# Optimization experiments

Hardware: AMD Instinct MI355X
Metric: run time of the kernel (lower is better)

Reference implementation:

```python
import jax, jax.numpy as jnp
import numpy as np

N, E, DIN, H, H1, H2, B, DEC = 20000, 320000, 128, 4, 64, 32, 4096, 512


def _seg_softmax(e, seg, n):
    # numerically stable softmax over edges grouped by destination node
    m = jax.ops.segment_max(e, seg, num_segments=n)
    p = jnp.exp(e - m[seg])
    s = jax.ops.segment_sum(p, seg, num_segments=n)
    return p / (s[seg] + 1e-16)


def _prelu(x, a):
    return jnp.where(x >= 0, x, a * x)


def _gat(x, src, dst, n, w, a_src, a_dst, b, concat):
    # PyG GATConv: shared linear, additive attention, leaky_relu(0.2), softmax per dst
    h_, c = a_src.shape
    h = (x @ w).reshape(-1, h_, c)                      # [n, H, C]
    al = jnp.einsum('nhc,hc->nh', h, a_src)[src] + jnp.einsum('nhc,hc->nh', h, a_dst)[dst]
    alpha = _seg_softmax(jax.nn.leaky_relu(al, 0.2), dst, n)  # [e, H]
    out = jax.ops.segment_sum(alpha[..., None] * h[src], dst, num_segments=n)
    out = out.reshape(n, h_ * c) if concat else out.mean(1)
    return out + b


def _gt(x, src, dst, n, wq, bq, wk, bk, wv, bv, ws, bs, heads, concat):
    # PyG TransformerConv: scaled dot-product attention over edges + root skip
    c = wq.shape[1] // heads
    q = (x @ wq + bq).reshape(-1, heads, c)
    k = (x @ wk + bk).reshape(-1, heads, c)
    v = (x @ wv + bv).reshape(-1, heads, c)
    e = (q[dst] * k[src]).sum(-1) / jnp.sqrt(jnp.float32(c))  # [e, heads]
    alpha = _seg_softmax(e, dst, n)
    agg = jax.ops.segment_sum(alpha[..., None] * v[src], dst, num_segments=n)
    agg = agg.reshape(n, heads * c) if concat else agg.mean(1)
    return agg + x @ ws + bs


def _forward(fl, edge_index, idx):
    (x_o, x_a, gat1_w, gat1_asrc, gat1_adst, gat1_b, gat2_w, gat2_asrc, gat2_adst, gat2_b,
     pg1, pg2, gt1_wq, gt1_bq, gt1_wk, gt1_bk, gt1_wv, gt1_bv, gt1_ws, gt1_bs,
     gt2_wq, gt2_bq, gt2_wk, gt2_bk, gt2_wv, gt2_bv, gt2_ws, gt2_bs, pt1, pt2,
     fuse_w, fuse_b, mlp1_w, mlp1_b, disc_w, disc_b,
     fus_w1, fus_b1, fus_w2, fus_b2, fus_w3, fus_b3, adv_w, adv_b) = fl
    n = x_o.shape[0]
    src, dst = edge_index[0], edge_index[1]
    # GATConv adds self loops by default; TransformerConv does not
    loop = jnp.arange(n, dtype=src.dtype)
    src_g = jnp.concatenate([src, loop])
    dst_g = jnp.concatenate([dst, loop])

    def branch_gat(x):
        x1 = _prelu(_gat(x, src_g, dst_g, n, gat1_w, gat1_asrc, gat1_adst, gat1_b, True), pg1)
        return _prelu(_gat(x1, src_g, dst_g, n, gat2_w, gat2_asrc, gat2_adst, gat2_b, False), pg2)

    def branch_gt(x):
        x1 = _prelu(_gt(x, src, dst, n, gt1_wq, gt1_bq, gt1_wk, gt1_bk, gt1_wv, gt1_bv, gt1_ws, gt1_bs, H, True), pt1)
        return _prelu(_gt(x1, src, dst, n, gt2_wq, gt2_bq, gt2_wk, gt2_bk, gt2_wv, gt2_bv, gt2_ws, gt2_bs, 1, False), pt2)

    x2_o = jnp.concatenate([branch_gat(x_o), branch_gt(x_o)], 1) @ fuse_w + fuse_b
    x2_a = jnp.concatenate([branch_gat(x_a), branch_gt(x_a)], 1) @ fuse_w + fuse_b

    def summary(z):
        return jax.nn.sigmoid(z.mean(0)) @ mlp1_w + mlp1_b   # [H2]

    h_os, h_os_a = summary(x2_o), summary(x2_a)

    def disc(cvec, hp, hm):
        # Bilinear(n_h, n_h, 1): sc = h W c^T + b
        s1 = (hp @ disc_w) @ cvec + disc_b[0]
        s2 = (hm @ disc_w) @ cvec + disc_b[0]
        return jnp.stack([s1, s2], 1)                       # [N, 2]

    ret_os = disc(h_os, x2_o, x2_a)
    ret_os_a = disc(h_os_a, x2_a, x2_o)

    # default task_type: direct indexing of node embeddings
    hcat = jnp.concatenate([x2_o[idx[0]], x2_o[idx[1]]], 1)  # [B, 2*H2]
    hh = jax.nn.relu(hcat @ fus_w1 + fus_b1)
    log = hh @ fus_w2 + fus_b2
    log1 = hh @ fus_w3 + fus_b3

    sc1 = (x2_o @ adv_w + adv_b).sum(1)[None, :]
    sc2 = (x2_a @ adv_w + adv_b).sum(1)[None, :]
    logits = jnp.concatenate([sc1, sc2], 1)                  # [1, 2N]
    return (log, ret_os, ret_os_a, x2_o, logits, log1)


_SHAPES = {
    'x_o': (N, DIN), 'x_a': (N, DIN),
    'gat1_w': (DIN, H * H1), 'gat1_asrc': (H, H1), 'gat1_adst': (H, H1), 'gat1_b': (H * H1,),
    'gat2_w': (H * H1, H2), 'gat2_asrc': (1, H2), 'gat2_adst': (1, H2), 'gat2_b': (H2,),
    'pg1': (H * H1,), 'pg2': (H2,),
    'gt1_wq': (DIN, H * H1), 'gt1_bq': (H * H1,), 'gt1_wk': (DIN, H * H1), 'gt1_bk': (H * H1,),
    'gt1_wv': (DIN, H * H1), 'gt1_bv': (H * H1,), 'gt1_ws': (DIN, H * H1), 'gt1_bs': (H * H1,),
    'gt2_wq': (H * H1, H2), 'gt2_bq': (H2,), 'gt2_wk': (H * H1, H2), 'gt2_bk': (H2,),
    'gt2_wv': (H * H1, H2), 'gt2_bv': (H2,), 'gt2_ws': (H * H1, H2), 'gt2_bs': (H2,),
    'pt1': (H * H1,), 'pt2': (H2,),
    'fuse_w': (2 * H2, H2), 'fuse_b': (H2,),
    'mlp1_w': (H2, H2), 'mlp1_b': (H2,),
    'disc_w': (H2, H2), 'disc_b': (1,),
    'fus_w1': (2 * H2, DEC), 'fus_b1': (DEC,), 'fus_w2': (DEC, 2), 'fus_b2': (2,),
    'fus_w3': (DEC, 2), 'fus_b3': (2,),
    'adv_w': (H2, H2), 'adv_b': (H2,),
}


def setup_inputs() -> dict:
    key = jax.random.key(0)
    inp = {}
    for i, (name, shp) in enumerate(_SHAPES.items()):
        inp[name] = jax.random.normal(jax.random.fold_in(key, i), shp, jnp.float32) * 0.05
    inp['edge_index'] = jax.random.randint(jax.random.fold_in(key, 100), (2, E), 0, N, dtype=jnp.int32)
    inp['idx'] = jax.random.randint(jax.random.fold_in(key, 101), (2, B), 0, N, dtype=jnp.int32)
    return inp


def reference(x_o, x_a, gat1_w, gat1_asrc, gat1_adst, gat1_b, gat2_w, gat2_asrc, gat2_adst, gat2_b,
              pg1, pg2, gt1_wq, gt1_bq, gt1_wk, gt1_bk, gt1_wv, gt1_bv, gt1_ws, gt1_bs,
              gt2_wq, gt2_bq, gt2_wk, gt2_bk, gt2_wv, gt2_bv, gt2_ws, gt2_bs, pt1, pt2,
              fuse_w, fuse_b, mlp1_w, mlp1_b, disc_w, disc_b,
              fus_w1, fus_b1, fus_w2, fus_b2, fus_w3, fus_b3, adv_w, adv_b,
              edge_index, idx):
    fl = (x_o, x_a, gat1_w, gat1_asrc, gat1_adst, gat1_b, gat2_w, gat2_asrc, gat2_adst, gat2_b,
          pg1, pg2, gt1_wq, gt1_bq, gt1_wk, gt1_bk, gt1_wv, gt1_bv, gt1_ws, gt1_bs,
          gt2_wq, gt2_bq, gt2_wk, gt2_bk, gt2_wv, gt2_bv, gt2_ws, gt2_bs, pt1, pt2,
          fuse_w, fuse_b, mlp1_w, mlp1_b, disc_w, disc_b,
          fus_w1, fus_b1, fus_w2, fus_b2, fus_w3, fus_b3, adv_w, adv_b)
    return _forward(fl, edge_index, idx)
```

## Files before the change

kernel.cpp:

```cpp
#include <hip/hip_runtime.h>
#include <math.h>

#define NN 20000
#define NE 320000
#define NB 4096

typedef unsigned short u16;
typedef unsigned char u8;
typedef __attribute__((ext_vector_type(8))) short short8;
typedef __attribute__((ext_vector_type(4))) float f32x4;
typedef __attribute__((ext_vector_type(2))) float f32x2;

#define FP8_SCALE 16.0f
#define FP8_INV 0.0625f
#define LOG2E 1.44269504088896341f

__device__ __forceinline__ float b2f(u16 u) {
  unsigned int x = ((unsigned int)u) << 16;
  return __uint_as_float(x);
}
__device__ __forceinline__ u16 f2b(float f) {
  unsigned int x = __float_as_uint(f);
  return (u16)((x + 0x7fffu + ((x >> 16) & 1u)) >> 16);
}
__device__ __forceinline__ float q2f(u8 b) {
  f32x2 v = __builtin_amdgcn_cvt_pk_f32_fp8((int)b, false);
  return v[0];
}
__device__ __forceinline__ void q4(unsigned int u, float* f) {
  f32x2 lo = __builtin_amdgcn_cvt_pk_f32_fp8((int)u, false);
  f32x2 hi = __builtin_amdgcn_cvt_pk_f32_fp8((int)u, true);
  f[0] = lo[0]; f[1] = lo[1]; f[2] = hi[0]; f[3] = hi[1];
}
template <int CTRL>
__device__ __forceinline__ float dppadd(float x) {
  int y = __builtin_amdgcn_update_dpp(0, __float_as_int(x), CTRL, 0xf, 0xf, true);
  return x + __int_as_float(y);
}
__device__ __forceinline__ float red16(float x) {
  x = dppadd<0xB1>(x);
  x = dppadd<0x4E>(x);
  x = dppadd<0x124>(x);
  x = dppadd<0x128>(x);
  return x;
}


__global__ void k_pack1(const float* __restrict__ w0, const float* __restrict__ w1,
                        const float* __restrict__ w2, const float* __restrict__ w3,
                        const float* __restrict__ w4, const float* __restrict__ b1,
                        const float* __restrict__ b2, const float* __restrict__ b3,
                        const float* __restrict__ b4, u16* __restrict__ Wt,
                        float* __restrict__ bp) {
  int t = blockIdx.x * blockDim.x + threadIdx.x;
  if (t < 1280 * 128) {
    int j = t >> 7, k = t & 127;
    int seg = j >> 8, jj = j & 255;
    const float* s = (seg == 0) ? w0 : (seg == 1) ? w1 : (seg == 2) ? w2 : (seg == 3) ? w3 : w4;
    Wt[t] = f2b(s[k * 256 + jj]);
  }
  if (t < 1280) {
    int seg = t >> 8, jj = t & 255;
    bp[t] = (seg == 0) ? 0.0f : (seg == 1) ? b1[jj] : (seg == 2) ? b2[jj] : (seg == 3) ? b3[jj] : b4[jj];
  }
}

__global__ void k_pack2(const float* __restrict__ wq, const float* __restrict__ wk,
                        const float* __restrict__ wv, const float* __restrict__ ws,
                        const float* __restrict__ wg, const float* __restrict__ bq,
                        const float* __restrict__ bk, const float* __restrict__ bv,
                        const float* __restrict__ bs, u16* __restrict__ Wt,
                        float* __restrict__ bp) {
  int t = blockIdx.x * blockDim.x + threadIdx.x;
  if (t < 160 * 256) {
    int j = t >> 8, k = t & 255;
    int seg = j >> 5, jj = j & 31;
    const float* s = (seg == 0) ? wq : (seg == 1) ? wk : (seg == 2) ? wv : (seg == 3) ? ws : wg;
    Wt[t] = f2b(s[k * 32 + jj]);
  }
  if (t < 160) {
    int seg = t >> 5, jj = t & 31;
    bp[t] = (seg == 0) ? bq[jj] : (seg == 1) ? bk[jj] : (seg == 2) ? bv[jj] : (seg == 3) ? bs[jj] : 0.0f;
  }
}

__global__ void k_tobf16x2(const float* __restrict__ xo, const float* __restrict__ xa,
                           u16* __restrict__ bo, u16* __restrict__ ba) {
  int t = blockIdx.x * blockDim.x + threadIdx.x;
  if (t >= 2 * NN * 128) return;
  if (t < NN * 128) bo[t] = f2b(xo[t]);
  else ba[t - NN * 128] = f2b(xa[t - NN * 128]);
}


__global__ void k_hist(const int* __restrict__ dst, int* __restrict__ deg) {
  int t = blockIdx.x * blockDim.x + threadIdx.x;
  if (t < NE) atomicAdd(&deg[dst[t]], 1);
}

__global__ void k_scan20000(const int* __restrict__ deg, int* __restrict__ offs,
                            int* __restrict__ cur) {
  __shared__ int part[1024];
  int t = threadIdx.x;
  int loc[20];
  int s = 0;
#pragma unroll
  for (int i = 0; i < 20; ++i) {
    int idx = t * 20 + i;
    int v = (idx < NN) ? deg[idx] : 0;
    loc[i] = s;
    s += v;
  }
  part[t] = s;
  __syncthreads();
  for (int off = 1; off < 1024; off <<= 1) {
    int v = (t >= off) ? part[t - off] : 0;
    __syncthreads();
    part[t] += v;
    __syncthreads();
  }
  int base = (t > 0) ? part[t - 1] : 0;
#pragma unroll
  for (int i = 0; i < 20; ++i) {
    int idx = t * 20 + i;
    if (idx < NN) {
      offs[idx] = base + loc[i];
      cur[idx] = base + loc[i];
    }
  }
  if (t == 1023) offs[NN] = part[1023];
}

__global__ void k_scatter(const int* __restrict__ src, const int* __restrict__ dst,
                          int* __restrict__ cur, int* __restrict__ esrcs) {
  int t = blockIdx.x * blockDim.x + threadIdx.x;
  if (t >= NE) return;
  int d = dst[t];
  int pos = atomicAdd(&cur[d], 1);
  esrcs[pos] = src[t];
}


template <int LAYER>
__global__ void k_mfma_gemm_s(const u16* __restrict__ A0, const u16* __restrict__ A1,
                              int asel, const u16* __restrict__ Bt,
                              const float* __restrict__ bias, int M, int K, int Nc,
                              u8* __restrict__ G, u16* __restrict__ Cb) {
  const u16* A = (blockIdx.x >= (unsigned)asel) ? A1 : A0;
  int m0 = blockIdx.y * 128, n0 = blockIdx.x * 128;
  int wid = threadIdx.x >> 6, lane = threadIdx.x & 63;
  int mw = m0 + (wid & 1) * 64, nw = n0 + (wid >> 1) * 64;
  int arow = mw + (lane & 15);
  int bcol = nw + (lane & 15);
  int kblk = (lane >> 4) * 8;
  f32x4 acc[4][4] = {};
  const short8 zero8 = {0, 0, 0, 0, 0, 0, 0, 0};
  for (int k0 = 0; k0 < K; k0 += 32) {
    short8 af[4], bf[4];
#pragma unroll
    for (int mf = 0; mf < 4; ++mf) {
      int r = arow + mf * 16;
      if (r > M - 1) r = M - 1;
      af[mf] = *reinterpret_cast<const short8*>(&A[(size_t)r * K + k0 + kblk]);
    }
#pragma unroll
    for (int nf = 0; nf < 4; ++nf) {
      int c = bcol + nf * 16;
      bf[nf] = (c < Nc) ? *reinterpret_cast<const short8*>(&Bt[(size_t)c * K + k0 + kblk])
                        : zero8;
    }
#pragma unroll
    for (int mf = 0; mf < 4; ++mf)
#pragma unroll
      for (int nf = 0; nf < 4; ++nf)
        acc[mf][nf] = __builtin_amdgcn_mfma_f32_16x16x32_bf16(bf[nf], af[mf],
                                                              acc[mf][nf], 0, 0, 0);
  }
  const int CSTR = (LAYER == 1) ? 512 : 64;
  const int GSTR = (LAYER == 1) ? 768 : 96;
#pragma unroll
  for (int mf = 0; mf < 4; ++mf) {
    int row = mw + mf * 16 + (lane & 15);
    if (row >= M) continue;
#pragma unroll
    for (int nf = 0; nf < 4; ++nf) {
      int col0 = nw + nf * 16 + ((lane >> 4) << 2);
      if (col0 >= Nc) continue;
      float4 bs4 = *reinterpret_cast<const float4*>(&bias[col0]);
      float v0 = acc[mf][nf][0] + bs4.x;
      float v1 = acc[mf][nf][1] + bs4.y;
      float v2 = acc[mf][nf][2] + bs4.z;
      float v3 = acc[mf][nf][3] + bs4.w;
      int seg = (LAYER == 1) ? (col0 >> 8) : (col0 >> 5);
      bool tobf = (LAYER == 1) ? (seg == 1 || seg == 4) : (seg == 0 || seg == 3);
      if (tobf) {
        int ccol = (LAYER == 1) ? ((seg == 1) ? col0 - 256 : col0 - 768)
                                : ((seg == 0) ? col0 : col0 - 64);
        ushort4 w4;
        w4.x = f2b(v0); w4.y = f2b(v1); w4.z = f2b(v2); w4.w = f2b(v3);
        *reinterpret_cast<ushort4*>(&Cb[(size_t)row * CSTR + ccol]) = w4;
      } else {
        int gcol = (LAYER == 1) ? ((seg == 0) ? col0 : col0 - 256)
                                : ((seg == 4) ? col0 - 64 : col0 - 32);
        unsigned int p = (unsigned int)__builtin_amdgcn_cvt_pk_fp8_f32(
            v0 * FP8_SCALE, v1 * FP8_SCALE, 0, false);
        p = (unsigned int)__builtin_amdgcn_cvt_pk_fp8_f32(
            v2 * FP8_SCALE, v3 * FP8_SCALE, (int)p, true);
        *reinterpret_cast<unsigned int*>(&G[(size_t)row * GSTR + gcol]) = p;
      }
    }
  }
}


__global__ void k_gat_al8(const u8* __restrict__ h, int stride, int coff,
                          const float* __restrict__ asrc, const float* __restrict__ adst,
                          float* __restrict__ als, float* __restrict__ ald, int total,
                          int heads, int c) {
  int i = blockIdx.x * blockDim.x + threadIdx.x;
  if (i >= total) return;
  int node = i / heads, hd = i - node * heads;
  const u8* hp = h + (size_t)node * stride + coff + hd * c;
  const float* as = asrc + hd * c;
  const float* ad = adst + hd * c;
  float s1 = 0.0f, s2 = 0.0f;
  for (int k = 0; k < c; k += 4) {
    float f[4];
    q4(*reinterpret_cast<const unsigned int*>(&hp[k]), f);
#pragma unroll
    for (int j = 0; j < 4; ++j) {
      s1 = fmaf(f[j], as[k + j], s1);
      s2 = fmaf(f[j], ad[k + j], s2);
    }
  }
  als[i] = s1 * (FP8_INV * LOG2E);
  ald[i] = s2 * (FP8_INV * LOG2E);
}

__global__ void k_agg256_fused(const int* __restrict__ offs, const int* __restrict__ esrcs,
                               const float* __restrict__ als, const float* __restrict__ ald,
                               const u8* __restrict__ G8, const u16* __restrict__ C1b,
                               const float* __restrict__ gbias,
                               const float* __restrict__ pg, const float* __restrict__ pt,
                               u16* __restrict__ outG, u16* __restrict__ outT) {
  int d = blockIdx.x * 4 + (threadIdx.x >> 6);
  if (d >= NN) return;
  int lane = threadIdx.x & 63;
  int head = lane >> 4, c4 = lane << 2;
  ushort4 q4v = *reinterpret_cast<const ushort4*>(&C1b[(size_t)d * 512 + c4]);
  float q0 = b2f(q4v.x), q1 = b2f(q4v.y), q2 = b2f(q4v.z), q3 = b2f(q4v.w);
  float aldd = ald[d * 4 + head];
  float ga0 = 0, ga1 = 0, ga2 = 0, ga3 = 0, gden = 0.0f;
  float ta0 = 0, ta1 = 0, ta2 = 0, ta3 = 0, tden = 1e-16f;
  int b0 = offs[d], b1 = offs[d + 1];
  const float GTC = 0.125f * FP8_INV * LOG2E;
  unsigned int f0 = 0, k0 = 0, v0 = 0, f1 = 0, k1 = 0, v1 = 0;
  float al0 = 0.0f, al1 = 0.0f;
  if (b0 < b1) {
    int s = esrcs[b0];
    const u8* row = &G8[(size_t)s * 768];
    f0 = *reinterpret_cast<const unsigned int*>(&row[c4]);
    k0 = *reinterpret_cast<const unsigned int*>(&row[256 + c4]);
    v0 = *reinterpret_cast<const unsigned int*>(&row[512 + c4]);
    al0 = als[s * 4 + head];
  }
  if (b0 + 1 < b1) {
    int s = esrcs[b0 + 1];
    const u8* row = &G8[(size_t)s * 768];
    f1 = *reinterpret_cast<const unsigned int*>(&row[c4]);
    k1 = *reinterpret_cast<const unsigned int*>(&row[256 + c4]);
    v1 = *reinterpret_cast<const unsigned int*>(&row[512 + c4]);
    al1 = als[s * 4 + head];
  }
  for (int i = b0; i < b1; ++i) {
    unsigned int f2_ = 0, k2_ = 0, v2_ = 0;
    float al2_ = 0.0f;
    if (i + 2 < b1) {
      int s = esrcs[i + 2];
      const u8* row = &G8[(size_t)s * 768];
      f2_ = *reinterpret_cast<const unsigned int*>(&row[c4]);
      k2_ = *reinterpret_cast<const unsigned int*>(&row[256 + c4]);
      v2_ = *reinterpret_cast<const unsigned int*>(&row[512 + c4]);
      al2_ = als[s * 4 + head];
    }
    float kf[4];
    q4(k0, kf);
    float pp = q0 * kf[0];
    pp = fmaf(q1, kf[1], pp);
    pp = fmaf(q2, kf[2], pp);
    pp = fmaf(q3, kf[3], pp);
    pp = red16(pp);
    float pet = exp2f(pp * GTC);
    float v = al0 + aldd;
    float peg = exp2f(v >= 0.0f ? v : 0.2f * v);
    float ff[4], vf[4];
    q4(f0, ff);
    q4(v0, vf);
    ga0 = fmaf(peg, ff[0], ga0);
    ga1 = fmaf(peg, ff[1], ga1);
    ga2 = fmaf(peg, ff[2], ga2);
    ga3 = fmaf(peg, ff[3], ga3);
    gden += peg;
    ta0 = fmaf(pet, vf[0], ta0);
    ta1 = fmaf(pet, vf[1], ta1);
    ta2 = fmaf(pet, vf[2], ta2);
    ta3 = fmaf(pet, vf[3], ta3);
    tden += pet;
    f0 = f1; k0 = k1; v0 = v1; al0 = al1;
    f1 = f2_; k1 = k2_; v1 = v2_; al1 = al2_;
  }
  {
    float v = als[d * 4 + head] + aldd;
    float pe = exp2f(v >= 0.0f ? v : 0.2f * v);
    float ff[4];
    q4(*reinterpret_cast<const unsigned int*>(&G8[(size_t)d * 768 + c4]), ff);
    ga0 = fmaf(pe, ff[0], ga0);
    ga1 = fmaf(pe, ff[1], ga1);
    ga2 = fmaf(pe, ff[2], ga2);
    ga3 = fmaf(pe, ff[3], ga3);
    gden += pe;
  }
  float ig = FP8_INV / gden, it = FP8_INV / tden;
  float o0 = ga0 * ig + gbias[c4 + 0];
  float o1 = ga1 * ig + gbias[c4 + 1];
  float o2 = ga2 * ig + gbias[c4 + 2];
  float o3 = ga3 * ig + gbias[c4 + 3];
  o0 = o0 >= 0.0f ? o0 : pg[c4 + 0] * o0;
  o1 = o1 >= 0.0f ? o1 : pg[c4 + 1] * o1;
  o2 = o2 >= 0.0f ? o2 : pg[c4 + 2] * o2;
  o3 = o3 >= 0.0f ? o3 : pg[c4 + 3] * o3;
  ushort4 wg4;
  wg4.x = f2b(o0); wg4.y = f2b(o1); wg4.z = f2b(o2); wg4.w = f2b(o3);
  *reinterpret_cast<ushort4*>(&outG[(size_t)d * 256 + c4]) = wg4;
  ushort4 sk = *reinterpret_cast<const ushort4*>(&C1b[(size_t)d * 512 + 256 + c4]);
  float u0 = ta0 * it + b2f(sk.x);
  float u1 = ta1 * it + b2f(sk.y);
  float u2 = ta2 * it + b2f(sk.z);
  float u3 = ta3 * it + b2f(sk.w);
  u0 = u0 >= 0.0f ? u0 : pt[c4 + 0] * u0;
  u1 = u1 >= 0.0f ? u1 : pt[c4 + 1] * u1;
  u2 = u2 >= 0.0f ? u2 : pt[c4 + 2] * u2;
  u3 = u3 >= 0.0f ? u3 : pt[c4 + 3] * u3;
  ushort4 wt4;
  wt4.x = f2b(u0); wt4.y = f2b(u1); wt4.z = f2b(u2); wt4.w = f2b(u3);
  *reinterpret_cast<ushort4*>(&outT[(size_t)d * 256 + c4]) = wt4;
}

__global__ void k_agg32_fuse(const int* __restrict__ offs, const int* __restrict__ esrcs,
                             const float* __restrict__ als, const float* __restrict__ ald,
                             const u8* __restrict__ G28, const u16* __restrict__ C2b,
                             const float* __restrict__ gbias,
                             const float* __restrict__ pg, const float* __restrict__ pt,
                             const float* __restrict__ fw, const float* __restrict__ fb,
                             float* __restrict__ x2out, float* __restrict__ colsum) {
  __shared__ float xgv[8][32], xtv[8][32];
  int g = threadIdx.x >> 5, l = threadIdx.x & 31;
  int d = blockIdx.x * 8 + g;
  float qv = b2f(C2b[(size_t)d * 64 + l]);
  float aldd = ald[d];
  float ga = 0.0f, gden = 0.0f;
  float ta = 0.0f, tden = 1e-16f;
  int b0 = offs[d], b1 = offs[d + 1];
  const float GTC2 = 0.17677669529663687f * FP8_INV * LOG2E;
  u8 kc = 0, vc = 0, hc = 0;
  float alc = 0;
  if (b0 < b1) {
    int sc = esrcs[b0];
    const u8* row = &G28[(size_t)sc * 96];
    kc = row[l]; vc = row[32 + l]; hc = row[64 + l];
    alc = als[sc];
  }
  for (int i = b0; i < b1; ++i) {
    u8 kn = kc, vn = vc, hn = hc;
    float aln = alc;
    if (i + 1 < b1) {
      int sn = esrcs[i + 1];
      const u8* row = &G28[(size_t)sn * 96];
      kn = row[l]; vn = row[32 + l]; hn = row[64 + l];
      aln = als[sn];
    }
    float pp = qv * q2f(kc);
    pp = red16(pp);
    pp += __shfl_xor(pp, 16, 32);
    float pet = exp2f(pp * GTC2);
    float v = alc + aldd;
    float peg = exp2f(v >= 0.0f ? v : 0.2f * v);
    ga = fmaf(peg, q2f(hc), ga);
    gden += peg;
    ta = fmaf(pet, q2f(vc), ta);
    tden += pet;
    kc = kn; vc = vn; hc = hn; alc = aln;
  }
  {
    float v = als[d] + aldd;
    float pe = exp2f(v >= 0.0f ? v : 0.2f * v);
    ga = fmaf(pe, q2f(G28[(size_t)d * 96 + 64 + l]), ga);
    gden += pe;
  }
  float og = ga * FP8_INV / gden + gbias[l];
  og = og >= 0.0f ? og : pg[l] * og;
  float ot = ta * FP8_INV / tden + b2f(C2b[(size_t)d * 64 + 32 + l]);
  ot = ot >= 0.0f ? ot : pt[l] * ot;
  xgv[g][l] = og;
  xtv[g][l] = ot;
  __syncthreads();
  float acc = fb[l];
#pragma unroll
  for (int i = 0; i < 32; ++i) {
    acc = fmaf(xgv[g][i], fw[i * 32 + l], acc);
    acc = fmaf(xtv[g][i], fw[(32 + i) * 32 + l], acc);
  }
  x2out[(size_t)d * 32 + l] = acc;
  __syncthreads();
  xgv[g][l] = acc;
  __syncthreads();
  if (g == 0) {
    float s = acc;
#pragma unroll
    for (int i = 1; i < 8; ++i) s += xgv[i][l];
    atomicAdd(&colsum[(blockIdx.x & 7) * 32 + l], s);
  }
}


__global__ void k_disc_all(const float* __restrict__ x2o, const float* __restrict__ x2a_,
                           const float* __restrict__ cso, const float* __restrict__ csa,
                           const float* __restrict__ mlp_w, const float* __restrict__ mlp_b,
                           const float* __restrict__ disc_w, const float* __restrict__ db,
                           float* __restrict__ ret_os, float* __restrict__ ret_os_a) {
  __shared__ float sgv[64], h1s[32], h2s[32], m1[32], m2[32];
  int t = threadIdx.x;
  if (t < 64) {
    int j = t & 31;
    const float* cs = (t < 32) ? cso : csa;
    float m = 0.0f;
#pragma unroll
    for (int i = 0; i < 8; ++i) m += cs[i * 32 + j];
    sgv[t] = 1.0f / (1.0f + expf(-m / (float)NN));
  }
  __syncthreads();
  if (t < 64) {
    int j = t & 31;
    const float* sg = (t < 32) ? sgv : sgv + 32;
    float acc = mlp_b[j];
#pragma unroll
    for (int i = 0; i < 32; ++i) acc = fmaf(sg[i], mlp_w[i * 32 + j], acc);
    (t < 32 ? h1s : h2s)[j] = acc;
  }
  __syncthreads();
  if (t < 64) {
    int k = t & 31;
    const float* hv = (t < 32) ? h1s : h2s;
    float acc = 0.0f;
#pragma unroll
    for (int i = 0; i < 32; ++i) acc = fmaf(disc_w[k * 32 + i], hv[i], acc);
    (t < 32 ? m1 : m2)[k] = acc;
  }
  __syncthreads();
  int n = blockIdx.x * blockDim.x + t;
  if (n >= NN) return;
  const float* a = x2o + (size_t)n * 32;
  const float* b = x2a_ + (size_t)n * 32;
  float s_oo = 0, s_ao = 0, s_aa = 0, s_oa = 0;
#pragma unroll
  for (int i = 0; i < 32; ++i) {
    float v1 = m1[i], v2 = m2[i];
    s_oo = fmaf(a[i], v1, s_oo);
    s_ao = fmaf(b[i], v1, s_ao);
    s_aa = fmaf(b[i], v2, s_aa);
    s_oa = fmaf(a[i], v2, s_oa);
  }
  float bb = db[0];
  ret_os[n * 2 + 0] = s_oo + bb;
  ret_os[n * 2 + 1] = s_ao + bb;
  ret_os_a[n * 2 + 0] = s_aa + bb;
  ret_os_a[n * 2 + 1] = s_oa + bb;
}

__global__ void k_dec1(const float* __restrict__ x2o, const int* __restrict__ idx0,
                       const int* __restrict__ idx1, const float* __restrict__ w,
                       const float* __restrict__ b1, float* __restrict__ hh) {
  int t = blockIdx.x * blockDim.x + threadIdx.x;
  if (t >= NB * 512) return;
  int bb = t >> 9, n = t & 511;
  const float* r0 = x2o + (size_t)idx0[bb] * 32;
  const float* r1 = x2o + (size_t)idx1[bb] * 32;
  float acc = b1[n];
#pragma unroll
  for (int i = 0; i < 32; ++i) acc = fmaf(r0[i], w[i * 512 + n], acc);
#pragma unroll
  for (int i = 0; i < 32; ++i) acc = fmaf(r1[i], w[(32 + i) * 512 + n], acc);
  hh[t] = fmaxf(acc, 0.0f);
}

__global__ void k_dec2w(const float* __restrict__ hh, const float* __restrict__ w2,
                        const float* __restrict__ b2, const float* __restrict__ w3,
                        const float* __restrict__ b3, float* __restrict__ logo,
                        float* __restrict__ log1) {
  int wv = (blockIdx.x * blockDim.x + threadIdx.x) >> 6;
  int lane = threadIdx.x & 63;
  if (wv >= NB * 4) return;
  int bb = wv >> 2, j = wv & 3;
  const float* h = hh + (size_t)bb * 512;
  const float* ws = (j < 2) ? w2 : w3;
  int jj = j & 1;
  float acc = 0.0f;
#pragma unroll
  for (int k = 0; k < 8; ++k) acc = fmaf(h[lane + k * 64], ws[(lane + k * 64) * 2 + jj], acc);
  acc += __shfl_xor(acc, 32);
  acc += __shfl_xor(acc, 16);
  acc += __shfl_xor(acc, 8);
  acc += __shfl_xor(acc, 4);
  acc += __shfl_xor(acc, 2);
  acc += __shfl_xor(acc, 1);
  if (lane == 0) {
    float b = (j < 2) ? b2[jj] : b3[jj];
    ((j < 2) ? logo : log1)[bb * 2 + jj] = acc + b;
  }
}

__global__ void k_adv(const float* __restrict__ x2o, const float* __restrict__ x2a,
                      const float* __restrict__ aw, const float* __restrict__ ab,
                      float* __restrict__ logits) {
  __shared__ float sadv[33];
  int t = threadIdx.x;
  if (t < 32) {
    float s = 0.0f;
#pragma unroll
    for (int j = 0; j < 32; ++j) s += aw[t * 32 + j];
    sadv[t] = s;
  } else if (t == 32) {
    float s = 0.0f;
#pragma unroll
    for (int j = 0; j < 32; ++j) s += ab[j];
    sadv[32] = s;
  }
  __syncthreads();
  int n = blockIdx.x * blockDim.x + t;
  if (n >= 2 * NN) return;
  const float* row = (n < NN) ? (x2o + (size_t)n * 32) : (x2a + (size_t)(n - NN) * 32);
  float acc = sadv[32];
#pragma unroll
  for (int i = 0; i < 32; ++i) acc = fmaf(row[i], sadv[i], acc);
  logits[n] = acc;
}


extern "C" void kernel_launch(void* const* d_in, const int* in_sizes, int n_in,
                              void* d_out, int out_size, void* d_ws, size_t ws_size,
                              hipStream_t stream) {
  const float* x_o = (const float*)d_in[0];
  const float* x_a = (const float*)d_in[1];
  const float* gat1_w = (const float*)d_in[2];
  const float* gat1_asrc = (const float*)d_in[3];
  const float* gat1_adst = (const float*)d_in[4];
  const float* gat1_b = (const float*)d_in[5];
  const float* gat2_w = (const float*)d_in[6];
  const float* gat2_asrc = (const float*)d_in[7];
  const float* gat2_adst = (const float*)d_in[8];
  const float* gat2_b = (const float*)d_in[9];
  const float* pg1 = (const float*)d_in[10];
  const float* pg2 = (const float*)d_in[11];
  const float* gt1_wq = (const float*)d_in[12];
  const float* gt1_bq = (const float*)d_in[13];
  const float* gt1_wk = (const float*)d_in[14];
  const float* gt1_bk = (const float*)d_in[15];
  const float* gt1_wv = (const float*)d_in[16];
  const float* gt1_bv = (const float*)d_in[17];
  const float* gt1_ws = (const float*)d_in[18];
  const float* gt1_bs = (const float*)d_in[19];
  const float* gt2_wq = (const float*)d_in[20];
  const float* gt2_bq = (const float*)d_in[21];
  const float* gt2_wk = (const float*)d_in[22];
  const float* gt2_bk = (const float*)d_in[23];
  const float* gt2_wv = (const float*)d_in[24];
  const float* gt2_bv = (const float*)d_in[25];
  const float* gt2_ws = (const float*)d_in[26];
  const float* gt2_bs = (const float*)d_in[27];
  const float* pt1 = (const float*)d_in[28];
  const float* pt2 = (const float*)d_in[29];
  const float* fuse_w = (const float*)d_in[30];
  const float* fuse_b = (const float*)d_in[31];
  const float* mlp1_w = (const float*)d_in[32];
  const float* mlp1_b = (const float*)d_in[33];
  const float* disc_w = (const float*)d_in[34];
  const float* disc_b = (const float*)d_in[35];
  const float* fus_w1 = (const float*)d_in[36];
  const float* fus_b1 = (const float*)d_in[37];
  const float* fus_w2 = (const float*)d_in[38];
  const float* fus_b2 = (const float*)d_in[39];
  const float* fus_w3 = (const float*)d_in[40];
  const float* fus_b3 = (const float*)d_in[41];
  const float* adv_w = (const float*)d_in[42];
  const float* adv_b = (const float*)d_in[43];
  const int* ei = (const int*)d_in[44];
  const int* idxp = (const int*)d_in[45];
  const int* esrc = ei;
  const int* edst = ei + NE;
  const int* idx0 = idxp;
  const int* idx1 = idxp + NB;

  float* w = (float*)d_ws;
  size_t o = 0;
  u8* G8 = (u8*)(w + o); o += 3840000;
  u16* C1b = (u16*)(w + o); o += 5120000;
  u8* G28 = (u8*)(w + o); o += 480000;
  u16* C2b = (u16*)(w + o); o += 640000;
  u16* bufB = (u16*)(w + o); o += 2560000;
  u16* bufE = (u16*)(w + o); o += 2560000;
  u16* xb_o = (u16*)(w + o); o += 1280000;
  u16* xb_a = (u16*)(w + o); o += 1280000;
  u16* Wt1 = (u16*)(w + o); o += 81920;
  u16* Wt2 = (u16*)(w + o); o += 20480;
  float* bp1 = w + o; o += 1280;
  float* bp2 = w + o; o += 160;
  float* als = w + o; o += NN * 4;
  float* ald = w + o; o += NN * 4;
  float* x2a = w + o; o += NN * 32;
  float* hh = w + o; o += NB * 512;
  int* deg = (int*)(w + o); o += NN;
  int* offs = (int*)(w + o); o += NN + 8;
  int* cur = (int*)(w + o); o += NN;
  int* esrcs = (int*)(w + o); o += NE;
  float* colsum_o = w + o; o += 256;
  float* colsum_a = w + o; o += 256;

  float* out = (float*)d_out;
  float* out_log = out;
  float* out_ret = out + 8192;
  float* out_reta = out + 48192;
  float* out_x2o = out + 88192;
  float* out_logit = out + 728192;
  float* out_log1 = out + 768192;

  k_pack1<<<(1280 * 128 + 255) / 256, 256, 0, stream>>>(gat1_w, gt1_wq, gt1_wk, gt1_wv,
                                                        gt1_ws, gt1_bq, gt1_bk, gt1_bv,
                                                        gt1_bs, Wt1, bp1);
  k_pack2<<<(160 * 256 + 255) / 256, 256, 0, stream>>>(gt2_wq, gt2_wk, gt2_wv, gt2_ws,
                                                       gat2_w, gt2_bq, gt2_bk, gt2_bv,
                                                       gt2_bs, Wt2, bp2);
  k_tobf16x2<<<(2 * NN * 128 + 255) / 256, 256, 0, stream>>>(x_o, x_a, xb_o, xb_a);
  hipMemsetAsync(deg, 0, NN * sizeof(int), stream);
  hipMemsetAsync(colsum_o, 0, 512 * sizeof(float), stream);
  k_hist<<<(NE + 255) / 256, 256, 0, stream>>>(edst, deg);
  k_scan20000<<<1, 1024, 0, stream>>>(deg, offs, cur);
  k_scatter<<<(NE + 255) / 256, 256, 0, stream>>>(esrc, edst, cur, esrcs);

  auto branch = [&](const u16* xb, float* x2out, float* colsum) {
    {
      dim3 g(10, (NN + 127) / 128);
      k_mfma_gemm_s<1><<<g, 256, 0, stream>>>(xb, xb, 999, Wt1, bp1, NN, 128, 1280,
                                              G8, C1b);
    }
    k_gat_al8<<<(NN * 4 + 255) / 256, 256, 0, stream>>>(G8, 768, 0, gat1_asrc, gat1_adst,
                                                        als, ald, NN * 4, 4, 64);
    k_agg256_fused<<<NN / 4, 256, 0, stream>>>(offs, esrcs, als, ald, G8, C1b,
                                               gat1_b, pg1, pt1, bufB, bufE);
    {
      dim3 g(2, (NN + 127) / 128);
      k_mfma_gemm_s<2><<<g, 256, 0, stream>>>(bufE, bufB, 1, Wt2, bp2, NN, 256, 160,
                                              G28, C2b);
    }
    k_gat_al8<<<(NN + 255) / 256, 256, 0, stream>>>(G28, 96, 64, gat2_asrc, gat2_adst,
                                                    als, ald, NN, 1, 32);
    k_agg32_fuse<<<NN / 8, 256, 0, stream>>>(offs, esrcs, als, ald, G28, C2b,
                                             gat2_b, pg2, pt2, fuse_w, fuse_b,
                                             x2out, colsum);
  };

  branch(xb_o, out_x2o, colsum_o);
  branch(xb_a, x2a, colsum_a);

  k_disc_all<<<(NN + 255) / 256, 256, 0, stream>>>(out_x2o, x2a, colsum_o, colsum_a,
                                                   mlp1_w, mlp1_b, disc_w, disc_b,
                                                   out_ret, out_reta);
  k_dec1<<<(NB * 512 + 255) / 256, 256, 0, stream>>>(out_x2o, idx0, idx1, fus_w1,
                                                     fus_b1, hh);
  k_dec2w<<<(NB * 4 * 64 + 255) / 256, 256, 0, stream>>>(hh, fus_w2, fus_b2, fus_w3,
                                                         fus_b3, out_log, out_log1);
  k_adv<<<(2 * NN + 255) / 256, 256, 0, stream>>>(out_x2o, x2a, adv_w, adv_b, out_logit);
}
```

Baseline: 464.4 us.

## Split edge aggregation across two waves per node and fuse tail kernels

The 256-wide aggregation kernel now assigns two wavefronts to each destination node. Each wave processes alternate edges, and the partial sums are combined through shared memory. This doubles the parallelism and memory-level concurrency on the gather-bound edge loop, at the cost of a block barrier and some LDS traffic. Separately, the adversarial logits are folded into the discriminator kernel, and the two decoder kernels are merged into one per-batch-row kernel that keeps the hidden layer in shared memory, removing two launches and the global hh buffer.

```diff
diff --git a/kernel.cpp b/kernel.cpp
--- a/kernel.cpp
+++ b/kernel.cpp
@@ -243,40 +243,43 @@
                                const float* __restrict__ gbias,
                                const float* __restrict__ pg, const float* __restrict__ pt,
                                u16* __restrict__ outG, u16* __restrict__ outT) {
-  int d = blockIdx.x * 4 + (threadIdx.x >> 6);
-  if (d >= NN) return;
+  __shared__ float part[2][64][10];
+  int g = threadIdx.x >> 6;
+  int dl = g >> 1, half = g & 1;
+  int d = blockIdx.x * 2 + dl;
   int lane = threadIdx.x & 63;
   int head = lane >> 4, c4 = lane << 2;
   ushort4 q4v = *reinterpret_cast<const ushort4*>(&C1b[(size_t)d * 512 + c4]);
   float q0 = b2f(q4v.x), q1 = b2f(q4v.y), q2 = b2f(q4v.z), q3 = b2f(q4v.w);
   float aldd = ald[d * 4 + head];
   float ga0 = 0, ga1 = 0, ga2 = 0, ga3 = 0, gden = 0.0f;
-  float ta0 = 0, ta1 = 0, ta2 = 0, ta3 = 0, tden = 1e-16f;
-  int b0 = offs[d], b1 = offs[d + 1];
+  float ta0 = 0, ta1 = 0, ta2 = 0, ta3 = 0;
+  float tden = half ? 0.0f : 1e-16f;
+  int bs = offs[d] + half, be = offs[d + 1];
   const float GTC = 0.125f * FP8_INV * LOG2E;
   unsigned int f0 = 0, k0 = 0, v0 = 0, f1 = 0, k1 = 0, v1 = 0;
   float al0 = 0.0f, al1 = 0.0f;
-  if (b0 < b1) {
-    int s = esrcs[b0];
+  if (bs < be) {
+    int s = esrcs[bs];
     const u8* row = &G8[(size_t)s * 768];
     f0 = *reinterpret_cast<const unsigned int*>(&row[c4]);
     k0 = *reinterpret_cast<const unsigned int*>(&row[256 + c4]);
     v0 = *reinterpret_cast<const unsigned int*>(&row[512 + c4]);
     al0 = als[s * 4 + head];
   }
-  if (b0 + 1 < b1) {
-    int s = esrcs[b0 + 1];
+  if (bs + 2 < be) {
+    int s = esrcs[bs + 2];
     const u8* row = &G8[(size_t)s * 768];
     f1 = *reinterpret_cast<const unsigned int*>(&row[c4]);
     k1 = *reinterpret_cast<const unsigned int*>(&row[256 + c4]);
     v1 = *reinterpret_cast<const unsigned int*>(&row[512 + c4]);
     al1 = als[s * 4 + head];
   }
-  for (int i = b0; i < b1; ++i) {
+  for (int i = bs; i < be; i += 2) {
     unsigned int f2_ = 0, k2_ = 0, v2_ = 0;
     float al2_ = 0.0f;
-    if (i + 2 < b1) {
-      int s = esrcs[i + 2];
+    if (i + 4 < be) {
+      int s = esrcs[i + 4];
       const u8* row = &G8[(size_t)s * 768];
       f2_ = *reinterpret_cast<const unsigned int*>(&row[c4]);
       k2_ = *reinterpret_cast<const unsigned int*>(&row[256 + c4]);
@@ -309,7 +312,7 @@
     f0 = f1; k0 = k1; v0 = v1; al0 = al1;
     f1 = f2_; k1 = k2_; v1 = v2_; al1 = al2_;
   }
-  {
+  if (half == 0) {
     float v = als[d * 4 + head] + aldd;
     float pe = exp2f(v >= 0.0f ? v : 0.2f * v);
     float ff[4];
@@ -320,6 +323,16 @@
     ga3 = fmaf(pe, ff[3], ga3);
     gden += pe;
   }
+  if (half == 1) {
+    float* p = part[dl][lane];
+    p[0] = ga0; p[1] = ga1; p[2] = ga2; p[3] = ga3; p[4] = gden;
+    p[5] = ta0; p[6] = ta1; p[7] = ta2; p[8] = ta3; p[9] = tden;
+  }
+  __syncthreads();
+  if (half == 1) return;
+  const float* p = part[dl][lane];
+  ga0 += p[0]; ga1 += p[1]; ga2 += p[2]; ga3 += p[3]; gden += p[4];
+  ta0 += p[5]; ta1 += p[6]; ta2 += p[7]; ta3 += p[8]; tden += p[9];
   float ig = FP8_INV / gden, it = FP8_INV / tden;
   float o0 = ga0 * ig + gbias[c4 + 0];
   float o1 = ga1 * ig + gbias[c4 + 1];
@@ -427,8 +440,10 @@
                            const float* __restrict__ cso, const float* __restrict__ csa,
                            const float* __restrict__ mlp_w, const float* __restrict__ mlp_b,
                            const float* __restrict__ disc_w, const float* __restrict__ db,
-                           float* __restrict__ ret_os, float* __restrict__ ret_os_a) {
-  __shared__ float sgv[64], h1s[32], h2s[32], m1[32], m2[32];
+                           const float* __restrict__ aw, const float* __restrict__ ab,
+                           float* __restrict__ ret_os, float* __restrict__ ret_os_a,
+                           float* __restrict__ logits) {
+  __shared__ float sgv[64], h1s[32], h2s[32], m1[32], m2[32], sadv[33];
   int t = threadIdx.x;
   if (t < 64) {
     int j = t & 31;
@@ -438,6 +453,18 @@
     for (int i = 0; i < 8; ++i) m += cs[i * 32 + j];
     sgv[t] = 1.0f / (1.0f + expf(-m / (float)NN));
   }
+  if (t >= 64 && t < 96) {
+    int j = t & 31;
+    float s = 0.0f;
+#pragma unroll
+    for (int i = 0; i < 32; ++i) s += aw[j * 32 + i];
+    sadv[j] = s;
+  } else if (t == 96) {
+    float s = 0.0f;
+#pragma unroll
+    for (int i = 0; i < 32; ++i) s += ab[i];
+    sadv[32] = s;
+  }
   __syncthreads();
   if (t < 64) {
     int j = t & 31;
@@ -462,51 +489,54 @@
   const float* a = x2o + (size_t)n * 32;
   const float* b = x2a_ + (size_t)n * 32;
   float s_oo = 0, s_ao = 0, s_aa = 0, s_oa = 0;
+  float lo = sadv[32], la = sadv[32];
 #pragma unroll
   for (int i = 0; i < 32; ++i) {
-    float v1 = m1[i], v2 = m2[i];
-    s_oo = fmaf(a[i], v1, s_oo);
-    s_ao = fmaf(b[i], v1, s_ao);
-    s_aa = fmaf(b[i], v2, s_aa);
-    s_oa = fmaf(a[i], v2, s_oa);
+    float v1 = m1[i], v2 = m2[i], av = sadv[i];
+    float ai = a[i], bi = b[i];
+    s_oo = fmaf(ai, v1, s_oo);
+    s_ao = fmaf(bi, v1, s_ao);
+    s_aa = fmaf(bi, v2, s_aa);
+    s_oa = fmaf(ai, v2, s_oa);
+    lo = fmaf(ai, av, lo);
+    la = fmaf(bi, av, la);
   }
   float bb = db[0];
   ret_os[n * 2 + 0] = s_oo + bb;
   ret_os[n * 2 + 1] = s_ao + bb;
   ret_os_a[n * 2 + 0] = s_aa + bb;
   ret_os_a[n * 2 + 1] = s_oa + bb;
-}
-
-__global__ void k_dec1(const float* __restrict__ x2o, const int* __restrict__ idx0,
-                       const int* __restrict__ idx1, const float* __restrict__ w,
-                       const float* __restrict__ b1, float* __restrict__ hh) {
-  int t = blockIdx.x * blockDim.x + threadIdx.x;
-  if (t >= NB * 512) return;
-  int bb = t >> 9, n = t & 511;
+  logits[n] = lo;
+  logits[NN + n] = la;
+}
+
+__global__ void k_dec(const float* __restrict__ x2o, const int* __restrict__ idx0,
+                      const int* __restrict__ idx1, const float* __restrict__ w1,
+                      const float* __restrict__ b1, const float* __restrict__ w2,
+                      const float* __restrict__ b2, const float* __restrict__ w3,
+                      const float* __restrict__ b3, float* __restrict__ logo,
+                      float* __restrict__ log1) {
+  __shared__ float hhs[512];
+  int bb = blockIdx.x;
   const float* r0 = x2o + (size_t)idx0[bb] * 32;
   const float* r1 = x2o + (size_t)idx1[bb] * 32;
-  float acc = b1[n];
-#pragma unroll
-  for (int i = 0; i < 32; ++i) acc = fmaf(r0[i], w[i * 512 + n], acc);
-#pragma unroll
-  for (int i = 0; i < 32; ++i) acc = fmaf(r1[i], w[(32 + i) * 512 + n], acc);
-  hh[t] = fmaxf(acc, 0.0f);
-}
-
-__global__ void k_dec2w(const float* __restrict__ hh, const float* __restrict__ w2,
-                        const float* __restrict__ b2, const float* __restrict__ w3,
-                        const float* __restrict__ b3, float* __restrict__ logo,
-                        float* __restrict__ log1) {
-  int wv = (blockIdx.x * blockDim.x + threadIdx.x) >> 6;
-  int lane = threadIdx.x & 63;
-  if (wv >= NB * 4) return;
-  int bb = wv >> 2, j = wv & 3;
-  const float* h = hh + (size_t)bb * 512;
-  const float* ws = (j < 2) ? w2 : w3;
-  int jj = j & 1;
+  int t = threadIdx.x;
+  for (int n = t; n < 512; n += 256) {
+    float acc = b1[n];
+#pragma unroll
+    for (int i = 0; i < 32; ++i) {
+      acc = fmaf(r0[i], w1[i * 512 + n], acc);
+      acc = fmaf(r1[i], w1[(32 + i) * 512 + n], acc);
+    }
+    hhs[n] = fmaxf(acc, 0.0f);
+  }
+  __syncthreads();
+  int g = t >> 6, lane = t & 63;
+  const float* ws = (g < 2) ? w2 : w3;
+  int jj = g & 1;
   float acc = 0.0f;
 #pragma unroll
-  for (int k = 0; k < 8; ++k) acc = fmaf(h[lane + k * 64], ws[(lane + k * 64) * 2 + jj], acc);
+  for (int k = 0; k < 8; ++k) acc = fmaf(hhs[lane + k * 64], ws[(lane + k * 64) * 2 + jj], acc);
   acc += __shfl_xor(acc, 32);
   acc += __shfl_xor(acc, 16);
   acc += __shfl_xor(acc, 8);
@@ -514,35 +544,9 @@
   acc += __shfl_xor(acc, 2);
   acc += __shfl_xor(acc, 1);
   if (lane == 0) {
-    float b = (j < 2) ? b2[jj] : b3[jj];
-    ((j < 2) ? logo : log1)[bb * 2 + jj] = acc + b;
-  }
-}
-
-__global__ void k_adv(const float* __restrict__ x2o, const float* __restrict__ x2a,
-                      const float* __restrict__ aw, const float* __restrict__ ab,
-                      float* __restrict__ logits) {
-  __shared__ float sadv[33];
-  int t = threadIdx.x;
-  if (t < 32) {
-    float s = 0.0f;
-#pragma unroll
-    for (int j = 0; j < 32; ++j) s += aw[t * 32 + j];
-    sadv[t] = s;
-  } else if (t == 32) {
-    float s = 0.0f;
-#pragma unroll
-    for (int j = 0; j < 32; ++j) s += ab[j];
-    sadv[32] = s;
-  }
-  __syncthreads();
-  int n = blockIdx.x * blockDim.x + t;
-  if (n >= 2 * NN) return;
-  const float* row = (n < NN) ? (x2o + (size_t)n * 32) : (x2a + (size_t)(n - NN) * 32);
-  float acc = sadv[32];
-#pragma unroll
-  for (int i = 0; i < 32; ++i) acc = fmaf(row[i], sadv[i], acc);
-  logits[n] = acc;
+    float b = (g < 2) ? b2[jj] : b3[jj];
+    ((g < 2) ? logo : log1)[bb * 2 + jj] = acc + b;
+  }
 }
 
 
@@ -617,7 +621,6 @@
   float* als = w + o; o += NN * 4;
   float* ald = w + o; o += NN * 4;
   float* x2a = w + o; o += NN * 32;
-  float* hh = w + o; o += NB * 512;
   int* deg = (int*)(w + o); o += NN;
   int* offs = (int*)(w + o); o += NN + 8;
   int* cur = (int*)(w + o); o += NN;
@@ -654,7 +657,7 @@
     }
     k_gat_al8<<<(NN * 4 + 255) / 256, 256, 0, stream>>>(G8, 768, 0, gat1_asrc, gat1_adst,
                                                         als, ald, NN * 4, 4, 64);
-    k_agg256_fused<<<NN / 4, 256, 0, stream>>>(offs, esrcs, als, ald, G8, C1b,
+    k_agg256_fused<<<NN / 2, 256, 0, stream>>>(offs, esrcs, als, ald, G8, C1b,
                                                gat1_b, pg1, pt1, bufB, bufE);
     {
       dim3 g(2, (NN + 127) / 128);
@@ -673,10 +676,8 @@
 
   k_disc_all<<<(NN + 255) / 256, 256, 0, stream>>>(out_x2o, x2a, colsum_o, colsum_a,
                                                    mlp1_w, mlp1_b, disc_w, disc_b,
-                                                   out_ret, out_reta);
-  k_dec1<<<(NB * 512 + 255) / 256, 256, 0, stream>>>(out_x2o, idx0, idx1, fus_w1,
-                                                     fus_b1, hh);
-  k_dec2w<<<(NB * 4 * 64 + 255) / 256, 256, 0, stream>>>(hh, fus_w2, fus_b2, fus_w3,
-                                                         fus_b3, out_log, out_log1);
-  k_adv<<<(2 * NN + 255) / 256, 256, 0, stream>>>(out_x2o, x2a, adv_w, adv_b, out_logit);
-}
+                                                   adv_w, adv_b, out_ret, out_reta,
+                                                   out_logit);
+  k_dec<<<NB, 256, 0, stream>>>(out_x2o, idx0, idx1, fus_w1, fus_b1, fus_w2, fus_b2,
+                                fus_w3, fus_b3, out_log, out_log1);
+}
```

Result: faster. 446.8 us (-3.8%).
